# Kernel optimization log

Hardware: AMD Instinct MI355X
Metric: run time of the kernel (lower is better)

## Reference

```python
import jax, jax.numpy as jnp
import numpy as np

HIDDEN = 128
ATT_DIM = 64
ATT_HOPS = 8
B, T, N = 64, 64, 64


def setup_inputs() -> dict:
    key = jax.random.key(0)
    k = jax.random.split(key, 7)
    node = jax.random.normal(k[0], (B, T, HIDDEN), dtype=jnp.float32)
    neigh = jax.random.normal(k[1], (B, N, T * HIDDEN), dtype=jnp.float32)
    neighbors_number = jax.random.randint(k[2], (B,), 1, 64, dtype=jnp.int64 if jax.config.jax_enable_x64 else jnp.int32)
    # nn.Linear params (torch layout: W [out, in])
    s = 1.0 / np.sqrt(HIDDEN)
    W1 = jax.random.uniform(k[3], (ATT_DIM, HIDDEN), jnp.float32, -s, s)
    b1 = jax.random.uniform(k[4], (ATT_DIM,), jnp.float32, -s, s)
    s2 = 1.0 / np.sqrt(ATT_DIM)
    W2 = jax.random.uniform(k[5], (ATT_HOPS, ATT_DIM), jnp.float32, -s2, s2)
    b2 = jax.random.uniform(k[6], (ATT_HOPS,), jnp.float32, -s2, s2)
    return {"node_rnn_output": node, "neigh_rnn_output": neigh,
            "neighbors_number": neighbors_number,
            "W1": W1, "b1": b1, "W2": W2, "b2": b2}


def reference(node_rnn_output, neigh_rnn_output, neighbors_number, W1, b1, W2, b2):
    Bb, Tt, D = node_rnn_output.shape
    Nn = neigh_rnn_output.shape[1]
    L = Nn * Tt
    neigh = neigh_rnn_output.reshape(Bb, L, D)            # [B, N*T, D]
    node_stacked = jnp.tile(node_rnn_output, (1, Nn, 1))  # [B, N*T, D]
    H = neigh * node_stacked                              # elementwise mul
    scale = jnp.sqrt(neighbors_number[0].astype(H.dtype))
    s1 = (jnp.einsum('bld,ad->bla', H, W1) + b1) / scale  # [B, L, att_dim]
    s2 = jnp.einsum('bla,ha->blh', jnp.tanh(s1), W2) + b2 # [B, L, hops]
    A = jax.nn.softmax(jnp.swapaxes(s2, 1, 2), axis=-1)   # [B, hops, L]
    BW = A.sum(axis=1).reshape(Bb, Nn, Tt)                # [B, N, T]
    AAT = jnp.einsum('bhl,bgl->bhg', A, A)                # [B, hops, hops]
    I = jnp.eye(A.shape[1], dtype=A.dtype)
    penal = jnp.sum((AAT - I) ** 2).reshape(1)            # sum of squared Frobenius norms
    return (BW, A, neigh, penal)
```

## Files before the change

kernel.cpp:

```cpp
#include <hip/hip_runtime.h>
#include <hip/hip_bf16.h>
#include <math.h>

#define HID 128
#define ATT 64
#define HOPS 8
#define T_ 64
#define N_ 64
#define B_ 64
#define L_ 4096

typedef __attribute__((ext_vector_type(8))) short bf16x8;
typedef __attribute__((ext_vector_type(4))) float f32x4;

static constexpr size_t OFF_A     = (size_t)B_ * N_ * T_;
static constexpr size_t OFF_NEIGH = OFF_A + (size_t)B_ * HOPS * L_;
static constexpr size_t OFF_PENAL = OFF_NEIGH + (size_t)B_ * L_ * HID;

__device__ __forceinline__ unsigned pkbf(float lo, float hi) {
    unsigned a = (unsigned)(unsigned short)__builtin_bit_cast(unsigned short, __float2bfloat16(lo));
    unsigned b = (unsigned)(unsigned short)__builtin_bit_cast(unsigned short, __float2bfloat16(hi));
    return a | (b << 16);
}
__device__ __forceinline__ short f2bf(float x) {
    return __builtin_bit_cast(short, __float2bfloat16(x));
}

typedef const __attribute__((address_space(1))) unsigned g1u32;
typedef __attribute__((address_space(3))) unsigned l3u32;

__device__ __forceinline__ void stage_strip(const float* src, unsigned* lds, int lane) {
    #pragma unroll
    for (int t = 0; t < 8; ++t) {
        __builtin_amdgcn_global_load_lds((g1u32*)((const unsigned*)src + t * 256 + lane * 4),
                                         (l3u32*)(lds + t * 256), 16, 0, 0);
    }
}

template<int WN> __device__ __forceinline__ void vwait() {
    if constexpr (WN == 8)       asm volatile("s_waitcnt vmcnt(8)" ::: "memory");
    else if constexpr (WN == 17) asm volatile("s_waitcnt vmcnt(17)" ::: "memory");
    else                         asm volatile("s_waitcnt vmcnt(9)" ::: "memory");
}

__device__ __forceinline__ void compute_strip(
    unsigned* hb, float* cd, float* s2p,
    const float nf[4][8], const bf16x8 wf[4][4], const bf16x8 wf2[2],
    const float b1v[4], float b2v, float inv_scale,
    int c, int g, int ro, int p)
{
    bf16x8 af[4];
    #pragma unroll
    for (int ks = 0; ks < 4; ++ks) {
        const float* hr = (const float*)hb + c * 128 + ks * 32 + g * 8;
        float4 a = *(const float4*)hr;
        float4 b = *(const float4*)(hr + 4);
        union { bf16x8 v; unsigned u[4]; } t;
        t.u[0] = pkbf(a.x * nf[ks][0], a.y * nf[ks][1]);
        t.u[1] = pkbf(a.z * nf[ks][2], a.w * nf[ks][3]);
        t.u[2] = pkbf(b.x * nf[ks][4], b.y * nf[ks][5]);
        t.u[3] = pkbf(b.z * nf[ks][6], b.w * nf[ks][7]);
        af[ks] = t.v;
    }
    float4 cr[8];
    #pragma unroll
    for (int j = 0; j < 8; ++j)
        cr[j] = *(const float4*)((const float*)hb + (2 * j + ro) * 128 + p * 4);
    #pragma unroll
    for (int j = 0; j < 8; ++j)
        *(float4*)(cd + (2 * j + ro) * 128 + p * 4) = cr[j];

    f32x4 acc[4];
    #pragma unroll
    for (int cf = 0; cf < 4; ++cf) acc[cf] = (f32x4){0.f, 0.f, 0.f, 0.f};
    #pragma unroll
    for (int cf = 0; cf < 4; ++cf) {
        #pragma unroll
        for (int ks = 0; ks < 4; ++ks)
            acc[cf] = __builtin_amdgcn_mfma_f32_16x16x32_bf16(af[ks], wf[cf][ks], acc[cf], 0, 0, 0);
    }

    asm volatile("" ::: "memory");

    short* thw = (short*)hb;
    #pragma unroll
    for (int cf = 0; cf < 4; ++cf) {
        #pragma unroll
        for (int jj = 0; jj < 4; ++jj) {
            float th = (acc[cf][jj] + b1v[cf]) * inv_scale;
            th = 1.0f - 2.0f / (__expf(2.0f * th) + 1.0f);
            thw[(g * 4 + jj) * 72 + cf * 16 + c] = f2bf(th);
        }
    }
    f32x4 acc2 = (f32x4){0.f, 0.f, 0.f, 0.f};
    #pragma unroll
    for (int ks2 = 0; ks2 < 2; ++ks2) {
        bf16x8 pa = *reinterpret_cast<const bf16x8*>(&thw[c * 72 + ks2 * 32 + g * 8]);
        acc2 = __builtin_amdgcn_mfma_f32_16x16x32_bf16(pa, wf2[ks2], acc2, 0, 0, 0);
    }
    if (c < 8) {
        float4 o;
        o.x = acc2[0] + b2v; o.y = acc2[1] + b2v;
        o.z = acc2[2] + b2v; o.w = acc2[3] + b2v;
        *(float4*)&s2p[(size_t)c * L_ + g * 4] = o;
    }
}

__global__ __launch_bounds__(256, 2)
void k1_mfma(const float* __restrict__ node, const float* __restrict__ neigh,
             const int* __restrict__ nnum, const float* __restrict__ W1,
             const float* __restrict__ b1, const float* __restrict__ W2,
             const float* __restrict__ b2, float* __restrict__ out)
{
    __shared__ __align__(16) unsigned sbuf[2][4][2048];

    const int tid  = threadIdx.x;
    const int w    = tid >> 6;
    const int lane = tid & 63;
    const int c    = lane & 15;
    const int g    = lane >> 4;
    const int ro   = lane >> 5;
    const int p    = lane & 31;

    const int Wv    = blockIdx.x * 4 + w;
    const int batch = Wv >> 5;
    const int widx  = Wv & 31;

    const float* nb0 = neigh + (size_t)batch * 524288 + (size_t)widx * 2048;
    float*       cd0 = out + OFF_NEIGH + (size_t)batch * 524288 + (size_t)widx * 2048;
    float*       s2b = out + OFF_A + (size_t)batch * 32768 + (size_t)widx * 16;

    unsigned* buf0 = &sbuf[0][w][0];
    unsigned* buf1 = &sbuf[1][w][0];

    stage_strip(nb0, buf0, lane);

    float nf[4][8];
    {
        const float* nd = node + (size_t)batch * 8192 + ((widx & 3) * 16 + c) * 128;
        #pragma unroll
        for (int ks = 0; ks < 4; ++ks) {
            float4 a = *(const float4*)(nd + ks * 32 + g * 8);
            float4 b = *(const float4*)(nd + ks * 32 + g * 8 + 4);
            nf[ks][0] = a.x; nf[ks][1] = a.y; nf[ks][2] = a.z; nf[ks][3] = a.w;
            nf[ks][4] = b.x; nf[ks][5] = b.y; nf[ks][6] = b.z; nf[ks][7] = b.w;
        }
    }
    bf16x8 wf[4][4];
    #pragma unroll
    for (int cf = 0; cf < 4; ++cf) {
        const float* wr = W1 + (cf * 16 + c) * 128;
        #pragma unroll
        for (int ks = 0; ks < 4; ++ks) {
            float4 a = *(const float4*)(wr + ks * 32 + g * 8);
            float4 b = *(const float4*)(wr + ks * 32 + g * 8 + 4);
            union { bf16x8 v; unsigned u[4]; } t;
            t.u[0] = pkbf(a.x, a.y); t.u[1] = pkbf(a.z, a.w);
            t.u[2] = pkbf(b.x, b.y); t.u[3] = pkbf(b.z, b.w);
            wf[cf][ks] = t.v;
        }
    }
    bf16x8 wf2[2];
    #pragma unroll
    for (int ks2 = 0; ks2 < 2; ++ks2) {
        union { bf16x8 v; unsigned u[4]; } t;
        #pragma unroll
        for (int i = 0; i < 4; ++i) {
            float lo = (c < 8) ? W2[c * 64 + ks2 * 32 + g * 8 + 2 * i]     : 0.f;
            float hi = (c < 8) ? W2[c * 64 + ks2 * 32 + g * 8 + 2 * i + 1] : 0.f;
            t.u[i] = pkbf(lo, hi);
        }
        wf2[ks2] = t.v;
    }
    float b1v[4];
    #pragma unroll
    for (int cf = 0; cf < 4; ++cf) b1v[cf] = b1[cf * 16 + c];
    const float b2v = (c < 8) ? b2[c] : 0.f;
    const float inv_scale = rsqrtf((float)nnum[0]);

    stage_strip(nb0 + 1 * 65536, buf1, lane);
    vwait<8>();
    compute_strip(buf0, cd0, s2b, nf, wf, wf2, b1v, b2v, inv_scale, c, g, ro, p);

    stage_strip(nb0 + 2 * 65536, buf0, lane);
    vwait<17>();
    compute_strip(buf1, cd0 + 1 * 65536, s2b + 512, nf, wf, wf2, b1v, b2v, inv_scale, c, g, ro, p);

    stage_strip(nb0 + 3 * 65536, buf1, lane);
    vwait<17>();
    compute_strip(buf0, cd0 + 2 * 65536, s2b + 1024, nf, wf, wf2, b1v, b2v, inv_scale, c, g, ro, p);

    stage_strip(nb0 + 4 * 65536, buf0, lane);
    vwait<17>();
    compute_strip(buf1, cd0 + 3 * 65536, s2b + 1536, nf, wf, wf2, b1v, b2v, inv_scale, c, g, ro, p);

    stage_strip(nb0 + 5 * 65536, buf1, lane);
    vwait<17>();
    compute_strip(buf0, cd0 + 4 * 65536, s2b + 2048, nf, wf, wf2, b1v, b2v, inv_scale, c, g, ro, p);

    stage_strip(nb0 + 6 * 65536, buf0, lane);
    vwait<17>();
    compute_strip(buf1, cd0 + 5 * 65536, s2b + 2560, nf, wf, wf2, b1v, b2v, inv_scale, c, g, ro, p);

    stage_strip(nb0 + 7 * 65536, buf1, lane);
    vwait<17>();
    compute_strip(buf0, cd0 + 6 * 65536, s2b + 3072, nf, wf, wf2, b1v, b2v, inv_scale, c, g, ro, p);

    vwait<9>();
    compute_strip(buf1, cd0 + 7 * 65536, s2b + 3584, nf, wf, wf2, b1v, b2v, inv_scale, c, g, ro, p);
}

__device__ __forceinline__ float waveMax(float v) {
    #pragma unroll
    for (int o = 32; o > 0; o >>= 1) v = fmaxf(v, __shfl_xor(v, o));
    return v;
}
__device__ __forceinline__ float waveSum(float v) {
    #pragma unroll
    for (int o = 32; o > 0; o >>= 1) v += __shfl_xor(v, o);
    return v;
}

__global__ __launch_bounds__(256)
void k2_stats(const float* __restrict__ out, float* __restrict__ stats, float* __restrict__ aat)
{
    const int bh = blockIdx.x;
    const int tid = threadIdx.x;
    if (bh == 0) {
        for (int i = tid; i < B_ * 36; i += 256) aat[i] = 0.f;
    }
    const float* row = out + OFF_A + (size_t)bh * L_;
    __shared__ float red[8];
    float m = -3.4e38f;
    for (int i = tid; i < L_; i += 256) m = fmaxf(m, row[i]);
    m = waveMax(m);
    if ((tid & 63) == 0) red[tid >> 6] = m;
    __syncthreads();
    const float M = fmaxf(fmaxf(red[0], red[1]), fmaxf(red[2], red[3]));
    float s = 0.0f;
    for (int i = tid; i < L_; i += 256) s += __expf(row[i] - M);
    s = waveSum(s);
    if ((tid & 63) == 0) red[4 + (tid >> 6)] = s;
    __syncthreads();
    if (tid == 0) {
        stats[bh * 2]     = M;
        stats[bh * 2 + 1] = red[4] + red[5] + red[6] + red[7];
    }
}

__global__ __launch_bounds__(256)
void k3_soft(float* __restrict__ out, const float* __restrict__ stats, float* __restrict__ aat)
{
    const int blk = blockIdx.x;
    const int b   = blk >> 2;
    const int l0  = (blk & 3) << 10;
    const int tid = threadIdx.x;
    float* A0 = out + OFF_A + (size_t)b * HOPS * L_;
    float* BW = out + (size_t)b * L_;
    float M[HOPS], R[HOPS];
    #pragma unroll
    for (int hh = 0; hh < HOPS; ++hh) {
        M[hh] = stats[(b * HOPS + hh) * 2];
        R[hh] = 1.0f / stats[(b * HOPS + hh) * 2 + 1];
    }
    float p[36];
    #pragma unroll
    for (int i = 0; i < 36; ++i) p[i] = 0.0f;
    for (int l = l0 + tid; l < l0 + 1024; l += 256) {
        float e[HOPS]; float srow = 0.0f;
        #pragma unroll
        for (int hh = 0; hh < HOPS; ++hh) {
            float v = __expf(A0[hh * L_ + l] - M[hh]) * R[hh];
            e[hh] = v; srow += v;
        }
        #pragma unroll
        for (int hh = 0; hh < HOPS; ++hh) A0[hh * L_ + l] = e[hh];
        BW[l] = srow;
        int i = 0;
        #pragma unroll
        for (int hh = 0; hh < HOPS; ++hh) {
            #pragma unroll
            for (int gg = hh; gg < HOPS; ++gg) { p[i] = fmaf(e[hh], e[gg], p[i]); ++i; }
        }
    }
    #pragma unroll
    for (int i = 0; i < 36; ++i) p[i] = waveSum(p[i]);
    __shared__ float red[4][36];
    const int wv = tid >> 6, ln = tid & 63;
    if (ln == 0) {
        #pragma unroll
        for (int i = 0; i < 36; ++i) red[wv][i] = p[i];
    }
    __syncthreads();
    if (tid < 36) {
        float s = red[0][tid] + red[1][tid] + red[2][tid] + red[3][tid];
        atomicAdd(&aat[b * 36 + tid], s);
    }
}

__global__ __launch_bounds__(256)
void k4_penal(const float* __restrict__ aat, float* __restrict__ out)
{
    const int tid = threadIdx.x;
    float s = 0.0f;
    for (int i = tid; i < B_ * 36; i += 256) {
        int r = i % 36;
        bool dg = (r == 0) | (r == 8) | (r == 15) | (r == 21) |
                  (r == 26) | (r == 30) | (r == 33) | (r == 35);
        float d = aat[i] - (dg ? 1.0f : 0.0f);
        float qd = d * d;
        s += dg ? qd : 2.0f * qd;
    }
    s = waveSum(s);
    __shared__ float red[4];
    if ((tid & 63) == 0) red[tid >> 6] = s;
    __syncthreads();
    if (tid == 0) out[OFF_PENAL] = red[0] + red[1] + red[2] + red[3];
}

extern "C" void kernel_launch(void* const* d_in, const int* in_sizes, int n_in,
                              void* d_out, int out_size, void* d_ws, size_t ws_size,
                              hipStream_t stream) {
    const float* node  = (const float*)d_in[0];
    const float* neigh = (const float*)d_in[1];
    const int*   nnum  = (const int*)d_in[2];
    const float* W1    = (const float*)d_in[3];
    const float* b1    = (const float*)d_in[4];
    const float* W2    = (const float*)d_in[5];
    const float* b2    = (const float*)d_in[6];
    float* out   = (float*)d_out;
    float* stats = (float*)d_ws;
    float* aat   = stats + 1024;

    k1_mfma <<<512, 256, 0, stream>>>(node, neigh, nnum, W1, b1, W2, b2, out);
    k2_stats<<<B_ * HOPS, 256, 0, stream>>>(out, stats, aat);
    k3_soft <<<256, 256, 0, stream>>>(out, stats, aat);
    k4_penal<<<1, 256, 0, stream>>>(aat, out);
}
```

Measured before the change: 89.64 us.

## Split neigh passthrough copy into dedicated copy blocks interleaved with MFMA blocks

The fused kernel no longer copies the neigh strip from LDS to the output inside each compute step. Instead, two of every three blocks do a plain float4 global-to-global copy of the neigh tensor, and the remaining blocks only run the MFMA attention scoring. The vmcnt waits are retuned because the compute waves no longer issue stores. This spreads the memory-bound copy across more blocks and removes store pressure from the pipelined compute waves. The cost is that neigh is read twice from global memory.

```diff
diff --git a/kernel.cpp b/kernel.cpp
--- a/kernel.cpp
+++ b/kernel.cpp
@@ -38,16 +38,15 @@
 }
 
 template<int WN> __device__ __forceinline__ void vwait() {
-    if constexpr (WN == 8)       asm volatile("s_waitcnt vmcnt(8)" ::: "memory");
-    else if constexpr (WN == 17) asm volatile("s_waitcnt vmcnt(17)" ::: "memory");
-    else                         asm volatile("s_waitcnt vmcnt(9)" ::: "memory");
+    if constexpr (WN == 8)      asm volatile("s_waitcnt vmcnt(8)" ::: "memory");
+    else if constexpr (WN == 9) asm volatile("s_waitcnt vmcnt(9)" ::: "memory");
+    else                        asm volatile("s_waitcnt vmcnt(1)" ::: "memory");
 }
 
 __device__ __forceinline__ void compute_strip(
-    unsigned* hb, float* cd, float* s2p,
+    unsigned* hb, float* s2p,
     const float nf[4][8], const bf16x8 wf[4][4], const bf16x8 wf2[2],
-    const float b1v[4], float b2v, float inv_scale,
-    int c, int g, int ro, int p)
+    const float b1v[4], float b2v, float inv_scale, int c, int g)
 {
     bf16x8 af[4];
     #pragma unroll
@@ -62,14 +61,6 @@
         t.u[3] = pkbf(b.z * nf[ks][6], b.w * nf[ks][7]);
         af[ks] = t.v;
     }
-    float4 cr[8];
-    #pragma unroll
-    for (int j = 0; j < 8; ++j)
-        cr[j] = *(const float4*)((const float*)hb + (2 * j + ro) * 128 + p * 4);
-    #pragma unroll
-    for (int j = 0; j < 8; ++j)
-        *(float4*)(cd + (2 * j + ro) * 128 + p * 4) = cr[j];
-
     f32x4 acc[4];
     #pragma unroll
     for (int cf = 0; cf < 4; ++cf) acc[cf] = (f32x4){0.f, 0.f, 0.f, 0.f};
@@ -79,9 +70,7 @@
         for (int ks = 0; ks < 4; ++ks)
             acc[cf] = __builtin_amdgcn_mfma_f32_16x16x32_bf16(af[ks], wf[cf][ks], acc[cf], 0, 0, 0);
     }
-
     asm volatile("" ::: "memory");
-
     short* thw = (short*)hb;
     #pragma unroll
     for (int cf = 0; cf < 4; ++cf) {
@@ -107,27 +96,43 @@
 }
 
 __global__ __launch_bounds__(256, 2)
-void k1_mfma(const float* __restrict__ node, const float* __restrict__ neigh,
-             const int* __restrict__ nnum, const float* __restrict__ W1,
-             const float* __restrict__ b1, const float* __restrict__ W2,
-             const float* __restrict__ b2, float* __restrict__ out)
+void k1_mix(const float* __restrict__ node, const float* __restrict__ neigh,
+            const int* __restrict__ nnum, const float* __restrict__ W1,
+            const float* __restrict__ b1, const float* __restrict__ W2,
+            const float* __restrict__ b2, float* __restrict__ out)
 {
     __shared__ __align__(16) unsigned sbuf[2][4][2048];
 
-    const int tid  = threadIdx.x;
+    const int tid = threadIdx.x;
+    const int bid = blockIdx.x;
+    const int a3  = bid / 3;
+    const int r3  = bid - a3 * 3;
+
+    if (r3 != 0) {
+        const int cid = a3 * 2 + (r3 - 1);
+        const float4* src = (const float4*)neigh + (size_t)cid * 8192 + tid;
+        float4*       dst = (float4*)(out + OFF_NEIGH) + (size_t)cid * 8192 + tid;
+        #pragma unroll
+        for (int grp = 0; grp < 4; ++grp) {
+            float4 v[8];
+            #pragma unroll
+            for (int j = 0; j < 8; ++j) v[j] = src[grp * 2048 + j * 256];
+            #pragma unroll
+            for (int j = 0; j < 8; ++j) dst[grp * 2048 + j * 256] = v[j];
+        }
+        return;
+    }
+
     const int w    = tid >> 6;
     const int lane = tid & 63;
     const int c    = lane & 15;
     const int g    = lane >> 4;
-    const int ro   = lane >> 5;
-    const int p    = lane & 31;
-
-    const int Wv    = blockIdx.x * 4 + w;
+
+    const int Wv    = a3 * 4 + w;
     const int batch = Wv >> 5;
     const int widx  = Wv & 31;
 
     const float* nb0 = neigh + (size_t)batch * 524288 + (size_t)widx * 2048;
-    float*       cd0 = out + OFF_NEIGH + (size_t)batch * 524288 + (size_t)widx * 2048;
     float*       s2b = out + OFF_A + (size_t)batch * 32768 + (size_t)widx * 16;
 
     unsigned* buf0 = &sbuf[0][w][0];
@@ -180,34 +185,34 @@
 
     stage_strip(nb0 + 1 * 65536, buf1, lane);
     vwait<8>();
-    compute_strip(buf0, cd0, s2b, nf, wf, wf2, b1v, b2v, inv_scale, c, g, ro, p);
+    compute_strip(buf0, s2b,        nf, wf, wf2, b1v, b2v, inv_scale, c, g);
 
     stage_strip(nb0 + 2 * 65536, buf0, lane);
-    vwait<17>();
-    compute_strip(buf1, cd0 + 1 * 65536, s2b + 512, nf, wf, wf2, b1v, b2v, inv_scale, c, g, ro, p);
+    vwait<9>();
+    compute_strip(buf1, s2b + 512,  nf, wf, wf2, b1v, b2v, inv_scale, c, g);
 
     stage_strip(nb0 + 3 * 65536, buf1, lane);
-    vwait<17>();
-    compute_strip(buf0, cd0 + 2 * 65536, s2b + 1024, nf, wf, wf2, b1v, b2v, inv_scale, c, g, ro, p);
+    vwait<9>();
+    compute_strip(buf0, s2b + 1024, nf, wf, wf2, b1v, b2v, inv_scale, c, g);
 
     stage_strip(nb0 + 4 * 65536, buf0, lane);
-    vwait<17>();
-    compute_strip(buf1, cd0 + 3 * 65536, s2b + 1536, nf, wf, wf2, b1v, b2v, inv_scale, c, g, ro, p);
+    vwait<9>();
+    compute_strip(buf1, s2b + 1536, nf, wf, wf2, b1v, b2v, inv_scale, c, g);
 
     stage_strip(nb0 + 5 * 65536, buf1, lane);
-    vwait<17>();
-    compute_strip(buf0, cd0 + 4 * 65536, s2b + 2048, nf, wf, wf2, b1v, b2v, inv_scale, c, g, ro, p);
+    vwait<9>();
+    compute_strip(buf0, s2b + 2048, nf, wf, wf2, b1v, b2v, inv_scale, c, g);
 
     stage_strip(nb0 + 6 * 65536, buf0, lane);
-    vwait<17>();
-    compute_strip(buf1, cd0 + 5 * 65536, s2b + 2560, nf, wf, wf2, b1v, b2v, inv_scale, c, g, ro, p);
+    vwait<9>();
+    compute_strip(buf1, s2b + 2560, nf, wf, wf2, b1v, b2v, inv_scale, c, g);
 
     stage_strip(nb0 + 7 * 65536, buf1, lane);
-    vwait<17>();
-    compute_strip(buf0, cd0 + 6 * 65536, s2b + 3072, nf, wf, wf2, b1v, b2v, inv_scale, c, g, ro, p);
-
-    vwait<9>();
-    compute_strip(buf1, cd0 + 7 * 65536, s2b + 3584, nf, wf, wf2, b1v, b2v, inv_scale, c, g, ro, p);
+    vwait<9>();
+    compute_strip(buf0, s2b + 3072, nf, wf, wf2, b1v, b2v, inv_scale, c, g);
+
+    vwait<1>();
+    compute_strip(buf1, s2b + 3584, nf, wf, wf2, b1v, b2v, inv_scale, c, g);
 }
 
 __device__ __forceinline__ float waveMax(float v) {
@@ -332,7 +337,7 @@
     float* stats = (float*)d_ws;
     float* aat   = stats + 1024;
 
-    k1_mfma <<<512, 256, 0, stream>>>(node, neigh, nnum, W1, b1, W2, b2, out);
+    k1_mix  <<<1536, 256, 0, stream>>>(node, neigh, nnum, W1, b1, W2, b2, out);
     k2_stats<<<B_ * HOPS, 256, 0, stream>>>(out, stats, aat);
     k3_soft <<<256, 256, 0, stream>>>(out, stats, aat);
     k4_penal<<<1, 256, 0, stream>>>(aat, out);
```

After: 102.6 us. +14.4%, slower.
